# Kernel optimization log

Hardware: AMD Instinct MI355X
Metric: run time of the kernel (lower is better)

## Reference

```python
import jax, jax.numpy as jnp
import numpy as np

B = 8192
D = 1024
NUM_CLASSES = 100


def setup_inputs() -> dict:
    key = jax.random.key(0)
    kx, ky = jax.random.split(key)
    x = jax.random.normal(kx, (B, D), dtype=jnp.float32)
    y = jax.random.randint(ky, (B,), 0, NUM_CLASSES, dtype=jnp.int64)
    return {"x": x, "y": y, "T": 1}


def reference(x, y, T):
    b = x.shape[0]
    # Pairwise Euclidean distances via Gram matrix (same math as
    # torch.norm(x[:,None]-x, dim=2) without the b*b*d intermediate).
    xn = jnp.sum(x * x, axis=1)                      # [b]
    d2 = xn[None, :] + xn[:, None] - 2.0 * (x @ x.T)  # [b, b]
    d2 = jnp.maximum(d2, 0.0)
    eye = jnp.eye(b, dtype=bool)
    # Diagonal is masked to -inf below; plug 1.0 to keep sqrt well-defined.
    dist = jnp.sqrt(jnp.where(eye, 1.0, d2))
    e_dist = -dist * T
    neg_inf = jnp.float32(-jnp.inf)
    # Denominator: all pairs except self.
    den_dist = jnp.where(eye, neg_inf, e_dist)
    # Numerator: same-label pairs except self.
    same = (y[None, :] == y[:, None]) & ~eye
    num_dist = jnp.where(same, e_dist, neg_inf)
    num = jax.nn.logsumexp(num_dist, axis=1)         # [b]
    den = jax.nn.logsumexp(den_dist, axis=1)         # [b]
    # Original fixup: anchors with no positives (num == -inf) contribute 0 to num;
    # den is re-indexed by isinf(num) AFTER num was zeroed, so den is unchanged.
    num = jnp.where(jnp.isinf(num), 0.0, num)
    return -jnp.mean(num - den)
```

## Files before the change

kernel.cpp:

```cpp
#include <hip/hip_runtime.h>
#include <hip/hip_bf16.h>
#include <stdint.h>

#define BN 8192
#define DK 1024
#define NT 16
#define NTILES 2080

typedef __attribute__((ext_vector_type(4))) float f32x4;
typedef __attribute__((ext_vector_type(2))) long long2v;

#define BAR() do { asm volatile("" ::: "memory"); __builtin_amdgcn_s_barrier(); asm volatile("" ::: "memory"); } while (0)

__device__ __forceinline__ unsigned int f2e4m3(float f) {
  const unsigned int u = __float_as_uint(f);
  const unsigned int sign = (u >> 24) & 0x80u;
  float a = fabsf(f);
  if (a >= 448.f) return sign | 0x7Eu;
  if (a < 0.015625f) {
    int m = (int)rintf(a * 512.f);
    return sign | (unsigned int)m;
  }
  unsigned int x = __float_as_uint(a);
  x += 0x7FFFFu + ((x >> 20) & 1u);
  const unsigned int e = (x >> 23) - 127u + 7u;
  const unsigned int m = (x >> 20) & 7u;
  return sign | (e << 4) | m;
}

__global__ __launch_bounds__(256) void snn_prep(const float* __restrict__ x,
                                                unsigned char* __restrict__ xb,
                                                float* __restrict__ xn,
                                                float* __restrict__ den,
                                                float* __restrict__ num,
                                                float* __restrict__ out) {
  const int row = blockIdx.x * 4 + (threadIdx.x >> 6);
  const int lane = threadIdx.x & 63;
  const float4* src = (const float4*)(x + (size_t)row * DK) + lane * 4;
  float s = 0.f;
  unsigned int pk[4];
#pragma unroll
  for (int i = 0; i < 4; ++i) {
    float4 v = src[i];
    s = fmaf(v.x, v.x, s); s = fmaf(v.y, v.y, s);
    s = fmaf(v.z, v.z, s); s = fmaf(v.w, v.w, s);
    pk[i] = f2e4m3(v.x) | (f2e4m3(v.y) << 8) | (f2e4m3(v.z) << 16) |
            (f2e4m3(v.w) << 24);
  }
  const int g = lane >> 2;
  const int c = lane & 3;
  uint4 o; o.x = pk[0]; o.y = pk[1]; o.z = pk[2]; o.w = pk[3];
  *(uint4*)(xb + (size_t)row * DK + g * 64 + ((c ^ ((row >> 1) & 3)) << 4)) = o;
#pragma unroll
  for (int m = 32; m >= 1; m >>= 1) s += __shfl_xor(s, m);
  if (lane == 0) {
    xn[row] = s;
    den[row] = 0.f;
    num[row] = 0.f;
    if (row == 0) out[0] = 0.f;
  }
}

__global__ __launch_bounds__(256, 3) void snn_main(
    const unsigned char* __restrict__ xb, const float* __restrict__ xn,
    const int* __restrict__ y, const unsigned int* __restrict__ Tp,
    float* __restrict__ den, float* __restrict__ num) {
  __shared__ __align__(16) unsigned char As[3][128 * 64];
  __shared__ __align__(16) unsigned char Bs[3][128 * 64];
  __shared__ float xnA[128], xnB[128];
  __shared__ int yA[128], yB[128];

  const int t = threadIdx.x;
  const int lane = t & 63;
  const int w = t >> 6;
  const int wr = w >> 1, wc = w & 1;
  const int l15 = lane & 15;
  const int lg = lane >> 4;

  const int bid = blockIdx.x;
  const int ts = (bid & 7) * (NTILES / 8) + (bid >> 3);
  int I = (int)(64.5f - sqrtf(64.5f * 64.5f - 2.0f * (float)ts));
  while (I > 0 && (64 * I - (I * (I - 1)) / 2) > ts) --I;
  while ((64 * (I + 1) - ((I + 1) * I) / 2) <= ts) ++I;
  const int J = I + (ts - (64 * I - (I * (I - 1)) / 2));
  const int r0 = I * 128, c0 = J * 128;
  const bool diag = (I == J);

  const unsigned int tu = *Tp;
  const float tf = (tu & 0x7f800000u) ? __uint_as_float(tu) : (float)(int)tu;

  if (t < 128) {
    xnA[t] = xn[r0 + t]; yA[t] = y[r0 + t];
    xnB[t] = xn[c0 + t]; yB[t] = y[c0 + t];
  }

  auto ISSUE = [&](int buf, int kt) {
#pragma unroll
    for (int i = 0; i < 2; ++i) {
      const int linear = i * 256 + t;
      const int row = linear >> 2;
      const int cg = linear & 3;
      const unsigned char* sa = xb + (size_t)(r0 + row) * DK + kt + cg * 16;
      const unsigned char* sb = xb + (size_t)(c0 + row) * DK + kt + cg * 16;
      __builtin_amdgcn_global_load_lds(
          (const __attribute__((address_space(1))) void*)sa,
          (__attribute__((address_space(3))) void*)(As[buf] + linear * 16), 16, 0, 0);
      __builtin_amdgcn_global_load_lds(
          (const __attribute__((address_space(1))) void*)sb,
          (__attribute__((address_space(3))) void*)(Bs[buf] + linear * 16), 16, 0, 0);
    }
  };

  f32x4 acc[4][4];
#pragma unroll
  for (int mi = 0; mi < 4; ++mi)
#pragma unroll
    for (int ni = 0; ni < 4; ++ni) acc[mi][ni] = (f32x4){0.f, 0.f, 0.f, 0.f};

  const int fro = (lg ^ ((l15 >> 1) & 3)) << 4;

  ISSUE(0, 0);
  ISSUE(1, 64);
  asm volatile("s_waitcnt vmcnt(4)" ::: "memory");
  BAR();

#pragma unroll
  for (int T = 0; T < NT; ++T) {
    const int rd = T % 3;
    const int st = (T + 2) % 3;
    long2v aF[4], bF[4];
#pragma unroll
    for (int mi = 0; mi < 4; ++mi) {
      const int row = wr * 64 + mi * 16 + l15;
      aF[mi] = *(const long2v*)(As[rd] + row * 64 + fro);
    }
#pragma unroll
    for (int ni = 0; ni < 4; ++ni) {
      const int row = wc * 64 + ni * 16 + l15;
      bF[ni] = *(const long2v*)(Bs[rd] + row * 64 + fro);
    }
    if (T + 2 < NT) {
      ISSUE(st, (T + 2) * 64);
      asm volatile("s_waitcnt vmcnt(4)" ::: "memory");
    } else if (T + 1 < NT) {
      asm volatile("s_waitcnt vmcnt(0)" ::: "memory");
    }
    __builtin_amdgcn_s_setprio(1);
#pragma unroll
    for (int kk = 0; kk < 2; ++kk)
#pragma unroll
      for (int mi = 0; mi < 4; ++mi)
#pragma unroll
        for (int ni = 0; ni < 4; ++ni)
          acc[mi][ni] = __builtin_amdgcn_mfma_f32_16x16x32_fp8_fp8(
              aF[mi][kk], bF[ni][kk], acc[mi][ni], 0, 0, 0);
    __builtin_amdgcn_s_setprio(0);
    BAR();
  }

  float cxn[4]; int cy[4];
#pragma unroll
  for (int ni = 0; ni < 4; ++ni) {
    const int c_l = wc * 64 + ni * 16 + l15;
    cxn[ni] = xnB[c_l]; cy[ni] = yB[c_l];
  }
#pragma unroll
  for (int mi = 0; mi < 4; ++mi) {
#pragma unroll
    for (int rg = 0; rg < 4; ++rg) {
      const int row_l = wr * 64 + mi * 16 + lg * 4 + rg;
      const int rG = r0 + row_l;
      const float rxn = xnA[row_l];
      const int ry = yA[row_l];
      float u = 0.f, av = 0.f;
#pragma unroll
      for (int ni = 0; ni < 4; ++ni) {
        const int cG = c0 + wc * 64 + ni * 16 + l15;
        const float a = acc[mi][ni][rg];
        const float d2 = fmaxf(rxn + cxn[ni] - 2.0f * a, 0.f);
        const float p = (rG == cG) ? 0.f : __expf(-sqrtf(d2) * tf);
        const float v = (ry == cy[ni]) ? -p : p;
        acc[mi][ni][rg] = v;
        u += v; av += fabsf(v);
      }
#pragma unroll
      for (int mm = 8; mm >= 1; mm >>= 1) {
        u += __shfl_xor(u, mm); av += __shfl_xor(av, mm);
      }
      if (l15 == 0) {
        atomicAdd(&den[rG], av);
        atomicAdd(&num[rG], 0.5f * (av - u));
      }
    }
  }
  if (!diag) {
#pragma unroll
    for (int ni = 0; ni < 4; ++ni) {
      float u = 0.f, av = 0.f;
#pragma unroll
      for (int mi = 0; mi < 4; ++mi)
#pragma unroll
        for (int rg = 0; rg < 4; ++rg) {
          const float v = acc[mi][ni][rg];
          u += v; av += fabsf(v);
        }
      u += __shfl_xor(u, 16); av += __shfl_xor(av, 16);
      u += __shfl_xor(u, 32); av += __shfl_xor(av, 32);
      if (lg == 0) {
        const int cG = c0 + wc * 64 + ni * 16 + l15;
        atomicAdd(&den[cG], av);
        atomicAdd(&num[cG], 0.5f * (av - u));
      }
    }
  }
}

__global__ __launch_bounds__(256) void snn_final(const float* __restrict__ den,
                                                 const float* __restrict__ num,
                                                 float* __restrict__ out) {
  __shared__ float red[256];
  const int t = threadIdx.x;
  const int r = blockIdx.x * 256 + t;
  const float sd = den[r], sn = num[r];
  const float d = logf(sd);
  const float n = (sn > 0.f) ? logf(sn) : 0.f;
  red[t] = d - n;
  __syncthreads();
  for (int s = 128; s >= 1; s >>= 1) {
    if (t < s) red[t] += red[t + s];
    __syncthreads();
  }
  if (t == 0) atomicAdd(out, red[0] * (1.0f / (float)BN));
}

extern "C" void kernel_launch(void* const* d_in, const int* in_sizes, int n_in,
                              void* d_out, int out_size, void* d_ws, size_t ws_size,
                              hipStream_t stream) {
  const float* x = (const float*)d_in[0];
  const int* y = (const int*)d_in[1];
  const unsigned int* Tp = (const unsigned int*)d_in[2];
  float* out = (float*)d_out;

  char* ws = (char*)d_ws;
  unsigned char* xb = (unsigned char*)ws;
  float* xn = (float*)(ws + (size_t)BN * DK);
  float* den = xn + BN;
  float* num = den + BN;

  snn_prep<<<dim3(BN / 4), dim3(256), 0, stream>>>(x, xb, xn, den, num, out);
  snn_main<<<dim3(NTILES), dim3(256), 0, stream>>>(xb, xn, y, Tp, den, num);
  snn_final<<<dim3(32), dim3(256), 0, stream>>>(den, num, out);
}
```

Before: 105.2 us.

## Load A fragments directly to registers and process two tiles per block

The A operand is no longer staged through LDS: each lane loads its fp8 A fragments straight from global memory into double-buffered registers, and only B uses the triple-buffered global_load_lds pipeline. The grid is halved so each block loops over two tiles, amortising setup and reducing LDS footprint. The s_setprio hints and the occupancy hint in launch_bounds are dropped. Direct global fragment loads are less coalesced and raise register pressure, and the wait counts had to be retuned for the new load mix.

```diff
diff --git a/kernel.cpp b/kernel.cpp
--- a/kernel.cpp
+++ b/kernel.cpp
@@ -4,8 +4,8 @@
 
 #define BN 8192
 #define DK 1024
-#define NT 16
 #define NTILES 2080
+#define GRID1 1040
 
 typedef __attribute__((ext_vector_type(4))) float f32x4;
 typedef __attribute__((ext_vector_type(2))) long long2v;
@@ -61,11 +61,10 @@
   }
 }
 
-__global__ __launch_bounds__(256, 3) void snn_main(
+__global__ __launch_bounds__(256) void snn_main(
     const unsigned char* __restrict__ xb, const float* __restrict__ xn,
     const int* __restrict__ y, const unsigned int* __restrict__ Tp,
     float* __restrict__ den, float* __restrict__ num) {
-  __shared__ __align__(16) unsigned char As[3][128 * 64];
   __shared__ __align__(16) unsigned char Bs[3][128 * 64];
   __shared__ float xnA[128], xnB[128];
   __shared__ int yA[128], yB[128];
@@ -77,139 +76,145 @@
   const int l15 = lane & 15;
   const int lg = lane >> 4;
 
-  const int bid = blockIdx.x;
-  const int ts = (bid & 7) * (NTILES / 8) + (bid >> 3);
-  int I = (int)(64.5f - sqrtf(64.5f * 64.5f - 2.0f * (float)ts));
-  while (I > 0 && (64 * I - (I * (I - 1)) / 2) > ts) --I;
-  while ((64 * (I + 1) - ((I + 1) * I) / 2) <= ts) ++I;
-  const int J = I + (ts - (64 * I - (I * (I - 1)) / 2));
-  const int r0 = I * 128, c0 = J * 128;
-  const bool diag = (I == J);
-
   const unsigned int tu = *Tp;
   const float tf = (tu & 0x7f800000u) ? __uint_as_float(tu) : (float)(int)tu;
 
-  if (t < 128) {
-    xnA[t] = xn[r0 + t]; yA[t] = y[r0 + t];
-    xnB[t] = xn[c0 + t]; yB[t] = y[c0 + t];
-  }
-
-  auto ISSUE = [&](int buf, int kt) {
-#pragma unroll
-    for (int i = 0; i < 2; ++i) {
-      const int linear = i * 256 + t;
-      const int row = linear >> 2;
-      const int cg = linear & 3;
-      const unsigned char* sa = xb + (size_t)(r0 + row) * DK + kt + cg * 16;
-      const unsigned char* sb = xb + (size_t)(c0 + row) * DK + kt + cg * 16;
-      __builtin_amdgcn_global_load_lds(
-          (const __attribute__((address_space(1))) void*)sa,
-          (__attribute__((address_space(3))) void*)(As[buf] + linear * 16), 16, 0, 0);
-      __builtin_amdgcn_global_load_lds(
-          (const __attribute__((address_space(1))) void*)sb,
-          (__attribute__((address_space(3))) void*)(Bs[buf] + linear * 16), 16, 0, 0);
-    }
-  };
-
-  f32x4 acc[4][4];
-#pragma unroll
-  for (int mi = 0; mi < 4; ++mi)
-#pragma unroll
-    for (int ni = 0; ni < 4; ++ni) acc[mi][ni] = (f32x4){0.f, 0.f, 0.f, 0.f};
-
   const int fro = (lg ^ ((l15 >> 1) & 3)) << 4;
 
-  ISSUE(0, 0);
-  ISSUE(1, 64);
-  asm volatile("s_waitcnt vmcnt(4)" ::: "memory");
-  BAR();
-
-#pragma unroll
-  for (int T = 0; T < NT; ++T) {
-    const int rd = T % 3;
-    const int st = (T + 2) % 3;
-    long2v aF[4], bF[4];
+  for (int half = 0; half < 2; ++half) {
+    const int bid = blockIdx.x + half * GRID1;
+    const int ts = (bid & 7) * (NTILES / 8) + (bid >> 3);
+    int I = (int)(64.5f - sqrtf(64.5f * 64.5f - 2.0f * (float)ts));
+    while (I > 0 && (64 * I - (I * (I - 1)) / 2) > ts) --I;
+    while ((64 * (I + 1) - ((I + 1) * I) / 2) <= ts) ++I;
+    const int J = I + (ts - (64 * I - (I * (I - 1)) / 2));
+    const int r0 = I * 128, c0 = J * 128;
+    const bool diag = (I == J);
+
+    BAR();
+    if (t < 128) {
+      xnA[t] = xn[r0 + t]; yA[t] = y[r0 + t];
+      xnB[t] = xn[c0 + t]; yB[t] = y[c0 + t];
+    }
+
+    const unsigned char* aBase[4];
+#pragma unroll
+    for (int mi = 0; mi < 4; ++mi)
+      aBase[mi] = xb + (size_t)(r0 + wr * 64 + mi * 16 + l15) * DK + fro;
+
+    auto ISSUEB = [&](int buf, int kt) {
+#pragma unroll
+      for (int i = 0; i < 2; ++i) {
+        const int linear = i * 256 + t;
+        const int row = linear >> 2;
+        const int cg = linear & 3;
+        const unsigned char* sb = xb + (size_t)(c0 + row) * DK + kt + cg * 16;
+        __builtin_amdgcn_global_load_lds(
+            (const __attribute__((address_space(1))) void*)sb,
+            (__attribute__((address_space(3))) void*)(Bs[buf] + linear * 16), 16, 0, 0);
+      }
+    };
+
+    f32x4 acc[4][4];
+#pragma unroll
+    for (int mi = 0; mi < 4; ++mi)
+#pragma unroll
+      for (int ni = 0; ni < 4; ++ni) acc[mi][ni] = (f32x4){0.f, 0.f, 0.f, 0.f};
+
+    long2v aR[2][4];
+
+    ISSUEB(0, 0);
+#pragma unroll
+    for (int mi = 0; mi < 4; ++mi)
+      aR[0][mi] = *(const long2v*)(aBase[mi]);
+    ISSUEB(1, 64);
+    asm volatile("s_waitcnt vmcnt(2)" ::: "memory");
+    asm volatile("s_waitcnt lgkmcnt(0)" ::: "memory");
+    BAR();
+
+#pragma unroll
+    for (int T = 0; T < 16; ++T) {
+      long2v bF[4];
+#pragma unroll
+      for (int ni = 0; ni < 4; ++ni)
+        bF[ni] = *(const long2v*)(Bs[T % 3] + (wc * 64 + ni * 16 + l15) * 64 + fro);
+      if (T < 15) {
+#pragma unroll
+        for (int mi = 0; mi < 4; ++mi)
+          aR[(T + 1) & 1][mi] = *(const long2v*)(aBase[mi] + (T + 1) * 64);
+      }
+      if (T + 2 < 16) {
+        ISSUEB((T + 2) % 3, (T + 2) * 64);
+        asm volatile("s_waitcnt vmcnt(6)" ::: "memory");
+      } else if (T == 14) {
+        asm volatile("s_waitcnt vmcnt(4)" ::: "memory");
+      } else {
+        asm volatile("s_waitcnt vmcnt(0)" ::: "memory");
+      }
+#pragma unroll
+      for (int kk = 0; kk < 2; ++kk)
+#pragma unroll
+        for (int mi = 0; mi < 4; ++mi)
+#pragma unroll
+          for (int ni = 0; ni < 4; ++ni)
+            acc[mi][ni] = __builtin_amdgcn_mfma_f32_16x16x32_fp8_fp8(
+                aR[T & 1][mi][kk], bF[ni][kk], acc[mi][ni], 0, 0, 0);
+      BAR();
+    }
+
+    float cxn[4]; int cy[4];
+#pragma unroll
+    for (int ni = 0; ni < 4; ++ni) {
+      const int c_l = wc * 64 + ni * 16 + l15;
+      cxn[ni] = xnB[c_l]; cy[ni] = yB[c_l];
+    }
 #pragma unroll
     for (int mi = 0; mi < 4; ++mi) {
-      const int row = wr * 64 + mi * 16 + l15;
-      aF[mi] = *(const long2v*)(As[rd] + row * 64 + fro);
-    }
-#pragma unroll
-    for (int ni = 0; ni < 4; ++ni) {
-      const int row = wc * 64 + ni * 16 + l15;
-      bF[ni] = *(const long2v*)(Bs[rd] + row * 64 + fro);
-    }
-    if (T + 2 < NT) {
-      ISSUE(st, (T + 2) * 64);
-      asm volatile("s_waitcnt vmcnt(4)" ::: "memory");
-    } else if (T + 1 < NT) {
-      asm volatile("s_waitcnt vmcnt(0)" ::: "memory");
-    }
-    __builtin_amdgcn_s_setprio(1);
-#pragma unroll
-    for (int kk = 0; kk < 2; ++kk)
-#pragma unroll
-      for (int mi = 0; mi < 4; ++mi)
-#pragma unroll
-        for (int ni = 0; ni < 4; ++ni)
-          acc[mi][ni] = __builtin_amdgcn_mfma_f32_16x16x32_fp8_fp8(
-              aF[mi][kk], bF[ni][kk], acc[mi][ni], 0, 0, 0);
-    __builtin_amdgcn_s_setprio(0);
-    BAR();
-  }
-
-  float cxn[4]; int cy[4];
-#pragma unroll
-  for (int ni = 0; ni < 4; ++ni) {
-    const int c_l = wc * 64 + ni * 16 + l15;
-    cxn[ni] = xnB[c_l]; cy[ni] = yB[c_l];
-  }
-#pragma unroll
-  for (int mi = 0; mi < 4; ++mi) {
-#pragma unroll
-    for (int rg = 0; rg < 4; ++rg) {
-      const int row_l = wr * 64 + mi * 16 + lg * 4 + rg;
-      const int rG = r0 + row_l;
-      const float rxn = xnA[row_l];
-      const int ry = yA[row_l];
-      float u = 0.f, av = 0.f;
+#pragma unroll
+      for (int rg = 0; rg < 4; ++rg) {
+        const int row_l = wr * 64 + mi * 16 + lg * 4 + rg;
+        const int rG = r0 + row_l;
+        const float rxn = xnA[row_l];
+        const int ry = yA[row_l];
+        float u = 0.f, av = 0.f;
+#pragma unroll
+        for (int ni = 0; ni < 4; ++ni) {
+          const int cG = c0 + wc * 64 + ni * 16 + l15;
+          const float a = acc[mi][ni][rg];
+          const float d2 = fmaxf(rxn + cxn[ni] - 2.0f * a, 0.f);
+          const float p = (rG == cG) ? 0.f : __expf(-sqrtf(d2) * tf);
+          const float v = (ry == cy[ni]) ? -p : p;
+          acc[mi][ni][rg] = v;
+          u += v; av += fabsf(v);
+        }
+#pragma unroll
+        for (int mm = 8; mm >= 1; mm >>= 1) {
+          u += __shfl_xor(u, mm); av += __shfl_xor(av, mm);
+        }
+        if (l15 == 0) {
+          atomicAdd(&den[rG], av);
+          atomicAdd(&num[rG], 0.5f * (av - u));
+        }
+      }
+    }
+    if (!diag) {
 #pragma unroll
       for (int ni = 0; ni < 4; ++ni) {
-        const int cG = c0 + wc * 64 + ni * 16 + l15;
-        const float a = acc[mi][ni][rg];
-        const float d2 = fmaxf(rxn + cxn[ni] - 2.0f * a, 0.f);
-        const float p = (rG == cG) ? 0.f : __expf(-sqrtf(d2) * tf);
-        const float v = (ry == cy[ni]) ? -p : p;
-        acc[mi][ni][rg] = v;
-        u += v; av += fabsf(v);
-      }
-#pragma unroll
-      for (int mm = 8; mm >= 1; mm >>= 1) {
-        u += __shfl_xor(u, mm); av += __shfl_xor(av, mm);
-      }
-      if (l15 == 0) {
-        atomicAdd(&den[rG], av);
-        atomicAdd(&num[rG], 0.5f * (av - u));
-      }
-    }
-  }
-  if (!diag) {
-#pragma unroll
-    for (int ni = 0; ni < 4; ++ni) {
-      float u = 0.f, av = 0.f;
-#pragma unroll
-      for (int mi = 0; mi < 4; ++mi)
-#pragma unroll
-        for (int rg = 0; rg < 4; ++rg) {
-          const float v = acc[mi][ni][rg];
-          u += v; av += fabsf(v);
-        }
-      u += __shfl_xor(u, 16); av += __shfl_xor(av, 16);
-      u += __shfl_xor(u, 32); av += __shfl_xor(av, 32);
-      if (lg == 0) {
-        const int cG = c0 + wc * 64 + ni * 16 + l15;
-        atomicAdd(&den[cG], av);
-        atomicAdd(&num[cG], 0.5f * (av - u));
+        float u = 0.f, av = 0.f;
+#pragma unroll
+        for (int mi = 0; mi < 4; ++mi)
+#pragma unroll
+          for (int rg = 0; rg < 4; ++rg) {
+            const float v = acc[mi][ni][rg];
+            u += v; av += fabsf(v);
+          }
+        u += __shfl_xor(u, 16); av += __shfl_xor(av, 16);
+        u += __shfl_xor(u, 32); av += __shfl_xor(av, 32);
+        if (lg == 0) {
+          const int cG = c0 + wc * 64 + ni * 16 + l15;
+          atomicAdd(&den[cG], av);
+          atomicAdd(&num[cG], 0.5f * (av - u));
+        }
       }
     }
   }
@@ -248,6 +253,6 @@
   float* num = den + BN;
 
   snn_prep<<<dim3(BN / 4), dim3(256), 0, stream>>>(x, xb, xn, den, num, out);
-  snn_main<<<dim3(NTILES), dim3(256), 0, stream>>>(xb, xn, y, Tp, den, num);
+  snn_main<<<dim3(GRID1), dim3(256), 0, stream>>>(xb, xn, y, Tp, den, num);
   snn_final<<<dim3(32), dim3(256), 0, stream>>>(den, num, out);
 }
```

Result: slower. 179.6 us (+70.8%).

## Switch FP8 GEMM to 32x32x64 scaled MFMA with wider fragments

Applied to the files above, without the earlier changes.

Replaces the 16x16x32 FP8 MFMA tiling (4x4 accumulators per wave) with the gfx950 scaled 32x32x64 f8f6f4 MFMA (2x2 accumulators of 16 floats). Each lane now loads two 16-byte LDS chunks per fragment, and the epilogue row/column mapping and shuffle reductions are rewritten for the 32-wide layout. The larger instruction cuts MFMA issue count and LDS fragment reads per k-step, but its output layout differs, so the epilogue indexing has to match it exactly. It also drops the last barrier and adds an lgkmcnt wait before the loop.

```diff
diff --git a/kernel.cpp b/kernel.cpp
--- a/kernel.cpp
+++ b/kernel.cpp
@@ -7,8 +7,9 @@
 #define NT 16
 #define NTILES 2080
 
-typedef __attribute__((ext_vector_type(4))) float f32x4;
-typedef __attribute__((ext_vector_type(2))) long long2v;
+typedef __attribute__((ext_vector_type(16))) float f32x16;
+typedef __attribute__((ext_vector_type(4))) int int32x4;
+typedef __attribute__((ext_vector_type(8))) int int32x8;
 
 #define BAR() do { asm volatile("" ::: "memory"); __builtin_amdgcn_s_barrier(); asm volatile("" ::: "memory"); } while (0)
 
@@ -74,8 +75,8 @@
   const int lane = t & 63;
   const int w = t >> 6;
   const int wr = w >> 1, wc = w & 1;
-  const int l15 = lane & 15;
-  const int lg = lane >> 4;
+  const int l31 = lane & 31;
+  const int hi = lane >> 5;
 
   const int bid = blockIdx.x;
   const int ts = (bid & 7) * (NTILES / 8) + (bid >> 3);
@@ -111,71 +112,91 @@
     }
   };
 
-  f32x4 acc[4][4];
-#pragma unroll
-  for (int mi = 0; mi < 4; ++mi)
-#pragma unroll
-    for (int ni = 0; ni < 4; ++ni) acc[mi][ni] = (f32x4){0.f, 0.f, 0.f, 0.f};
-
-  const int fro = (lg ^ ((l15 >> 1) & 3)) << 4;
+  f32x16 acc[2][2];
+#pragma unroll
+  for (int mi = 0; mi < 2; ++mi)
+#pragma unroll
+    for (int ni = 0; ni < 2; ++ni)
+#pragma unroll
+      for (int r = 0; r < 16; ++r) acc[mi][ni][r] = 0.f;
+
+  int aOffLo[2], aOffHi[2], bOffLo[2], bOffHi[2];
+#pragma unroll
+  for (int mi = 0; mi < 2; ++mi) {
+    const int row = wr * 64 + mi * 32 + l31;
+    const int s = (row >> 1) & 3;
+    aOffLo[mi] = row * 64 + (((2 * hi) ^ s) << 4);
+    aOffHi[mi] = row * 64 + (((2 * hi + 1) ^ s) << 4);
+  }
+#pragma unroll
+  for (int ni = 0; ni < 2; ++ni) {
+    const int row = wc * 64 + ni * 32 + l31;
+    const int s = (row >> 1) & 3;
+    bOffLo[ni] = row * 64 + (((2 * hi) ^ s) << 4);
+    bOffHi[ni] = row * 64 + (((2 * hi + 1) ^ s) << 4);
+  }
 
   ISSUE(0, 0);
   ISSUE(1, 64);
   asm volatile("s_waitcnt vmcnt(4)" ::: "memory");
+  asm volatile("s_waitcnt lgkmcnt(0)" ::: "memory");
   BAR();
 
 #pragma unroll
   for (int T = 0; T < NT; ++T) {
-    const int rd = T % 3;
-    const int st = (T + 2) % 3;
-    long2v aF[4], bF[4];
-#pragma unroll
-    for (int mi = 0; mi < 4; ++mi) {
-      const int row = wr * 64 + mi * 16 + l15;
-      aF[mi] = *(const long2v*)(As[rd] + row * 64 + fro);
-    }
-#pragma unroll
-    for (int ni = 0; ni < 4; ++ni) {
-      const int row = wc * 64 + ni * 16 + l15;
-      bF[ni] = *(const long2v*)(Bs[rd] + row * 64 + fro);
+    const unsigned char* bufA = As[T % 3];
+    const unsigned char* bufB = Bs[T % 3];
+    int32x8 aV[2], bV[2];
+#pragma unroll
+    for (int mi = 0; mi < 2; ++mi) {
+      int32x4 lo = *(const int32x4*)(bufA + aOffLo[mi]);
+      int32x4 hq = *(const int32x4*)(bufA + aOffHi[mi]);
+      aV[mi][0] = lo[0]; aV[mi][1] = lo[1]; aV[mi][2] = lo[2]; aV[mi][3] = lo[3];
+      aV[mi][4] = hq[0]; aV[mi][5] = hq[1]; aV[mi][6] = hq[2]; aV[mi][7] = hq[3];
+    }
+#pragma unroll
+    for (int ni = 0; ni < 2; ++ni) {
+      int32x4 lo = *(const int32x4*)(bufB + bOffLo[ni]);
+      int32x4 hq = *(const int32x4*)(bufB + bOffHi[ni]);
+      bV[ni][0] = lo[0]; bV[ni][1] = lo[1]; bV[ni][2] = lo[2]; bV[ni][3] = lo[3];
+      bV[ni][4] = hq[0]; bV[ni][5] = hq[1]; bV[ni][6] = hq[2]; bV[ni][7] = hq[3];
     }
     if (T + 2 < NT) {
-      ISSUE(st, (T + 2) * 64);
+      ISSUE((T + 2) % 3, (T + 2) * 64);
       asm volatile("s_waitcnt vmcnt(4)" ::: "memory");
-    } else if (T + 1 < NT) {
+    } else if (T == NT - 2) {
       asm volatile("s_waitcnt vmcnt(0)" ::: "memory");
     }
     __builtin_amdgcn_s_setprio(1);
 #pragma unroll
-    for (int kk = 0; kk < 2; ++kk)
-#pragma unroll
-      for (int mi = 0; mi < 4; ++mi)
-#pragma unroll
-        for (int ni = 0; ni < 4; ++ni)
-          acc[mi][ni] = __builtin_amdgcn_mfma_f32_16x16x32_fp8_fp8(
-              aF[mi][kk], bF[ni][kk], acc[mi][ni], 0, 0, 0);
+    for (int mi = 0; mi < 2; ++mi)
+#pragma unroll
+      for (int ni = 0; ni < 2; ++ni)
+        acc[mi][ni] = __builtin_amdgcn_mfma_scale_f32_32x32x64_f8f6f4(
+            aV[mi], bV[ni], acc[mi][ni], 0, 0,
+            0, 0x7F7F7F7F, 0, 0x7F7F7F7F);
     __builtin_amdgcn_s_setprio(0);
-    BAR();
-  }
-
-  float cxn[4]; int cy[4];
-#pragma unroll
-  for (int ni = 0; ni < 4; ++ni) {
-    const int c_l = wc * 64 + ni * 16 + l15;
+    if (T < NT - 1) BAR();
+  }
+
+  float cxn[2]; int cy[2];
+#pragma unroll
+  for (int ni = 0; ni < 2; ++ni) {
+    const int c_l = wc * 64 + ni * 32 + l31;
     cxn[ni] = xnB[c_l]; cy[ni] = yB[c_l];
   }
 #pragma unroll
-  for (int mi = 0; mi < 4; ++mi) {
-#pragma unroll
-    for (int rg = 0; rg < 4; ++rg) {
-      const int row_l = wr * 64 + mi * 16 + lg * 4 + rg;
+  for (int mi = 0; mi < 2; ++mi) {
+#pragma unroll
+    for (int rg = 0; rg < 16; ++rg) {
+      const int row_l = wr * 64 + mi * 32 + (rg & 3) + ((rg >> 2) << 3) + (hi << 2);
       const int rG = r0 + row_l;
       const float rxn = xnA[row_l];
       const int ry = yA[row_l];
       float u = 0.f, av = 0.f;
 #pragma unroll
-      for (int ni = 0; ni < 4; ++ni) {
-        const int cG = c0 + wc * 64 + ni * 16 + l15;
+      for (int ni = 0; ni < 2; ++ni) {
+        const int cG = c0 + wc * 64 + ni * 32 + l31;
         const float a = acc[mi][ni][rg];
         const float d2 = fmaxf(rxn + cxn[ni] - 2.0f * a, 0.f);
         const float p = (rG == cG) ? 0.f : __expf(-sqrtf(d2) * tf);
@@ -184,10 +205,10 @@
         u += v; av += fabsf(v);
       }
 #pragma unroll
-      for (int mm = 8; mm >= 1; mm >>= 1) {
+      for (int mm = 16; mm >= 1; mm >>= 1) {
         u += __shfl_xor(u, mm); av += __shfl_xor(av, mm);
       }
-      if (l15 == 0) {
+      if (l31 == 0) {
         atomicAdd(&den[rG], av);
         atomicAdd(&num[rG], 0.5f * (av - u));
       }
@@ -195,19 +216,18 @@
   }
   if (!diag) {
 #pragma unroll
-    for (int ni = 0; ni < 4; ++ni) {
+    for (int ni = 0; ni < 2; ++ni) {
       float u = 0.f, av = 0.f;
 #pragma unroll
-      for (int mi = 0; mi < 4; ++mi)
-#pragma unroll
-        for (int rg = 0; rg < 4; ++rg) {
+      for (int mi = 0; mi < 2; ++mi)
+#pragma unroll
+        for (int rg = 0; rg < 16; ++rg) {
           const float v = acc[mi][ni][rg];
           u += v; av += fabsf(v);
         }
-      u += __shfl_xor(u, 16); av += __shfl_xor(av, 16);
       u += __shfl_xor(u, 32); av += __shfl_xor(av, 32);
-      if (lg == 0) {
-        const int cG = c0 + wc * 64 + ni * 16 + l15;
+      if (hi == 0) {
+        const int cG = c0 + wc * 64 + ni * 32 + l31;
         atomicAdd(&den[cG], av);
         atomicAdd(&num[cG], 0.5f * (av - u));
       }
```

Result: slower. 344.2 us (+227.3%).
